# Optimization experiments

Hardware: AMD Instinct MI355X
Metric: run time of the kernel (lower is better)

## Reference

```python
import jax, jax.numpy as jnp
import numpy as np

N = 8192
E = 262144
D_IN = 256
D_OUT = 256
EPS = 1e-05


def setup_inputs() -> dict:
    key = jax.random.key(0)
    kx, ke0, ke1, kw = jax.random.split(key, 4)
    x = jax.random.normal(kx, (N, D_IN), dtype=jnp.float32)
    edge_index = jnp.stack([
        jax.random.randint(ke0, (E,), 0, N, dtype=jnp.int64),
        jax.random.randint(ke1, (E,), 0, N, dtype=jnp.int64),
    ], axis=0)
    # nn.Linear(in, out, bias=False): weight shape [out, in], kaiming-uniform-ish init
    bound = 1.0 / np.sqrt(D_IN)
    W = jax.random.uniform(kw, (D_OUT, D_IN), dtype=jnp.float32, minval=-bound, maxval=bound)
    return {"x": x, "edge_index": edge_index, "W": W}


def reference(x, edge_index, W):
    n = x.shape[0]
    # A_hat = I with edges set to 1 (set semantics; duplicates harmless)
    A_hat = jnp.eye(n, dtype=x.dtype).at[edge_index[0], edge_index[1]].set(1.0)
    # D_hat = diag(1/sqrt(rowsum + eps)); A_norm = D_hat @ A_hat @ D_hat
    d_inv = 1.0 / jnp.sqrt(A_hat.sum(axis=1) + EPS)  # [N]
    A_norm = d_inv[:, None] * A_hat * d_inv[None, :]  # [N, N]
    h = x @ W.T  # [N, D_OUT]
    return jax.nn.relu(A_norm @ h)
```

## Files before the change

kernel.cpp:

```cpp
#include <hip/hip_runtime.h>
#include <hip/hip_bf16.h>
#include <math.h>

#define N_NODES 8192
#define DIM 256
#define WPR 256
#define MAXD 128
#define EPS 1e-5f

typedef __attribute__((ext_vector_type(8))) short bf16x8;
typedef __attribute__((ext_vector_type(4))) float f32x4;

__device__ inline float bfhi(unsigned u) { return __uint_as_float(u & 0xffff0000u); }
__device__ inline float bflo(unsigned u) { return __uint_as_float(u << 16); }

#define NX4 (N_NODES * DIM / 4)
#define NW4 (DIM * DIM / 4)
__global__ __launch_bounds__(256) void prep(const float* __restrict__ x,
                                            const float* __restrict__ W,
                                            const int* __restrict__ erows,
                                            const int* __restrict__ ecols,
                                            __hip_bfloat16* __restrict__ xb,
                                            __hip_bfloat16* __restrict__ Wb,
                                            unsigned* __restrict__ bitmap,
                                            int* __restrict__ degree,
                                            int* __restrict__ cols, int E) {
    int t = blockIdx.x * 256 + threadIdx.x;
    if (t < NX4 + NW4) {
        const float* src = (t < NX4) ? x : W;
        __hip_bfloat16* dst = (t < NX4) ? xb : Wb;
        size_t off = (size_t)((t < NX4) ? t : (t - NX4)) * 4;
        float4 v = *(const float4*)(src + off);
        union { __hip_bfloat16 h[4]; uint2 u; } p;
        p.h[0] = __float2bfloat16(v.x);
        p.h[1] = __float2bfloat16(v.y);
        p.h[2] = __float2bfloat16(v.z);
        p.h[3] = __float2bfloat16(v.w);
        *(uint2*)(dst + off) = p.u;
        return;
    }
    int e = t - (NX4 + NW4);
    if (e >= E + N_NODES) return;
    int r, c;
    if (e < E) { r = erows[e]; c = ecols[e]; }
    else       { r = e - E;    c = r; }
    unsigned bit = 1u << (c & 31);
    unsigned old = atomicOr(&bitmap[(size_t)r * WPR + (c >> 5)], bit);
    if (!(old & bit)) {
        int p = atomicAdd(&degree[r], 1);
        cols[(size_t)r * MAXD + p] = c;
    }
}

__global__ __launch_bounds__(256) void gemm_mfma(const short* __restrict__ xb,
                                                 const short* __restrict__ Wb,
                                                 const int* __restrict__ degree,
                                                 __hip_bfloat16* __restrict__ g) {
    int wave = threadIdx.x >> 6;
    int lane = threadIdx.x & 63;
    int bm = blockIdx.x * 64 + wave * 16;
    int bn = blockIdx.y * 64;
    int quad = lane >> 4;
    int l16 = lane & 15;
    f32x4 acc[4] = {};
    const short* arow = xb + (size_t)(bm + l16) * DIM + quad * 8;
#pragma unroll
    for (int k0 = 0; k0 < DIM; k0 += 32) {
        bf16x8 a = *(const bf16x8*)(arow + k0);
#pragma unroll
        for (int s = 0; s < 4; s++) {
            bf16x8 b = *(const bf16x8*)(Wb + (size_t)(bn + s * 16 + l16) * DIM + k0 + quad * 8);
            acc[s] = __builtin_amdgcn_mfma_f32_16x16x32_bf16(a, b, acc[s], 0, 0, 0);
        }
    }
#pragma unroll
    for (int r = 0; r < 4; r++) {
        int m = bm + quad * 4 + r;
        float s0 = rsqrtf((float)degree[m] + EPS);
#pragma unroll
        for (int s = 0; s < 4; s++)
            g[(size_t)m * DIM + bn + s * 16 + l16] = __float2bfloat16(s0 * acc[s][r]);
    }
}

__global__ __launch_bounds__(256) void aggregate(const int* __restrict__ degree,
                                                 const int* __restrict__ cols,
                                                 const uint2* __restrict__ g2,
                                                 float* __restrict__ out) {
    int wave = threadIdx.x >> 6;
    int lane = threadIdx.x & 63;
    int row = blockIdx.x * 4 + wave;
    int n = degree[row];
    const int* cl = cols + (size_t)row * MAXD;
    float s0[4] = {0.f,0.f,0.f,0.f}, s1[4] = {0.f,0.f,0.f,0.f};
    float s2[4] = {0.f,0.f,0.f,0.f}, s3[4] = {0.f,0.f,0.f,0.f};
    float s4[4] = {0.f,0.f,0.f,0.f}, s5[4] = {0.f,0.f,0.f,0.f};
    float s6[4] = {0.f,0.f,0.f,0.f}, s7[4] = {0.f,0.f,0.f,0.f};
    int i = 0;
    for (; i + 8 <= n; i += 8) {
        int4 ja = *(const int4*)(cl + i);
        int4 jb = *(const int4*)(cl + i + 4);
        uint2 u0 = g2[(size_t)ja.x * 64 + lane];
        uint2 u1 = g2[(size_t)ja.y * 64 + lane];
        uint2 u2 = g2[(size_t)ja.z * 64 + lane];
        uint2 u3 = g2[(size_t)ja.w * 64 + lane];
        uint2 u4 = g2[(size_t)jb.x * 64 + lane];
        uint2 u5 = g2[(size_t)jb.y * 64 + lane];
        uint2 u6 = g2[(size_t)jb.z * 64 + lane];
        uint2 u7 = g2[(size_t)jb.w * 64 + lane];
        s0[0] += bflo(u0.x); s0[1] += bfhi(u0.x); s0[2] += bflo(u0.y); s0[3] += bfhi(u0.y);
        s1[0] += bflo(u1.x); s1[1] += bfhi(u1.x); s1[2] += bflo(u1.y); s1[3] += bfhi(u1.y);
        s2[0] += bflo(u2.x); s2[1] += bfhi(u2.x); s2[2] += bflo(u2.y); s2[3] += bfhi(u2.y);
        s3[0] += bflo(u3.x); s3[1] += bfhi(u3.x); s3[2] += bflo(u3.y); s3[3] += bfhi(u3.y);
        s4[0] += bflo(u4.x); s4[1] += bfhi(u4.x); s4[2] += bflo(u4.y); s4[3] += bfhi(u4.y);
        s5[0] += bflo(u5.x); s5[1] += bfhi(u5.x); s5[2] += bflo(u5.y); s5[3] += bfhi(u5.y);
        s6[0] += bflo(u6.x); s6[1] += bfhi(u6.x); s6[2] += bflo(u6.y); s6[3] += bfhi(u6.y);
        s7[0] += bflo(u7.x); s7[1] += bfhi(u7.x); s7[2] += bflo(u7.y); s7[3] += bfhi(u7.y);
    }
    for (; i + 4 <= n; i += 4) {
        int4 ja = *(const int4*)(cl + i);
        uint2 u0 = g2[(size_t)ja.x * 64 + lane];
        uint2 u1 = g2[(size_t)ja.y * 64 + lane];
        uint2 u2 = g2[(size_t)ja.z * 64 + lane];
        uint2 u3 = g2[(size_t)ja.w * 64 + lane];
        s0[0] += bflo(u0.x); s0[1] += bfhi(u0.x); s0[2] += bflo(u0.y); s0[3] += bfhi(u0.y);
        s1[0] += bflo(u1.x); s1[1] += bfhi(u1.x); s1[2] += bflo(u1.y); s1[3] += bfhi(u1.y);
        s2[0] += bflo(u2.x); s2[1] += bfhi(u2.x); s2[2] += bflo(u2.y); s2[3] += bfhi(u2.y);
        s3[0] += bflo(u3.x); s3[1] += bfhi(u3.x); s3[2] += bflo(u3.y); s3[3] += bfhi(u3.y);
    }
    for (; i < n; i++) {
        uint2 u = g2[(size_t)cl[i] * 64 + lane];
        s0[0] += bflo(u.x); s0[1] += bfhi(u.x); s0[2] += bflo(u.y); s0[3] += bfhi(u.y);
    }
    float sc = rsqrtf((float)n + EPS);
    float4 o;
    o.x = fmaxf(sc * (((s0[0]+s1[0])+(s2[0]+s3[0])) + ((s4[0]+s5[0])+(s6[0]+s7[0]))), 0.f);
    o.y = fmaxf(sc * (((s0[1]+s1[1])+(s2[1]+s3[1])) + ((s4[1]+s5[1])+(s6[1]+s7[1]))), 0.f);
    o.z = fmaxf(sc * (((s0[2]+s1[2])+(s2[2]+s3[2])) + ((s4[2]+s5[2])+(s6[2]+s7[2]))), 0.f);
    o.w = fmaxf(sc * (((s0[3]+s1[3])+(s2[3]+s3[3])) + ((s4[3]+s5[3])+(s6[3]+s7[3]))), 0.f);
    *(float4*)(out + (size_t)row * DIM + lane * 4) = o;
}

extern "C" void kernel_launch(void* const* d_in, const int* in_sizes, int n_in,
                              void* d_out, int out_size, void* d_ws, size_t ws_size,
                              hipStream_t stream) {
    const float* x = (const float*)d_in[0];
    const int* ei = (const int*)d_in[1];
    const float* W = (const float*)d_in[2];
    float* out = (float*)d_out;
    int E = in_sizes[1] / 2;

    unsigned char* ws = (unsigned char*)d_ws;
    size_t off = 0;
    unsigned* bitmap = (unsigned*)(ws + off); off += (size_t)N_NODES * WPR * 4;
    int* degree = (int*)(ws + off);           off += (size_t)N_NODES * 4;
    int* cols = (int*)(ws + off);             off += (size_t)N_NODES * MAXD * 4;
    __hip_bfloat16* xb = (__hip_bfloat16*)(ws + off); off += (size_t)N_NODES * DIM * 2;
    __hip_bfloat16* Wb = (__hip_bfloat16*)(ws + off); off += (size_t)DIM * DIM * 2;
    __hip_bfloat16* g = (__hip_bfloat16*)(ws + off);  off += (size_t)N_NODES * DIM * 2;

    hipMemsetAsync(bitmap, 0, (size_t)N_NODES * WPR * 4 + (size_t)N_NODES * 4, stream);
    int units = NX4 + NW4 + E + N_NODES;
    prep<<<(units + 255) / 256, 256, 0, stream>>>(x, W, ei, ei + E, xb, Wb, bitmap, degree, cols, E);
    dim3 ggrid(N_NODES / 64, DIM / 64);
    gemm_mfma<<<ggrid, 256, 0, stream>>>((const short*)xb, (const short*)Wb, degree, g);
    aggregate<<<N_NODES / 4, 256, 0, stream>>>(degree, cols, (const uint2*)g, out);
}
```

Measured before the change: 118.1 us.

## Fuse bf16 conversion and workspace zeroing into GEMM, move column scaling to aggregate

Replaces the separate memset and the prep kernel's x/W bf16 conversion with a GEMM that converts fp32 tiles to bf16 in shared memory and zeroes the bitmap and degree buffers in a grid-stride loop. Edge scattering becomes its own kernel that runs after the GEMM, so the GEMM no longer needs degree and the source-side normalisation moves into aggregate as a per-neighbour rsqrt FMA. This removes the bf16 copies of x and W and one launch. In exchange, aggregate does extra gathered degree loads and rsqrt work, and the GEMM's conversion is repeated across column blocks.

```diff
diff --git a/kernel.cpp b/kernel.cpp
--- a/kernel.cpp
+++ b/kernel.cpp
@@ -7,6 +7,7 @@
 #define WPR 256
 #define MAXD 128
 #define EPS 1e-5f
+#define ZWORDS (N_NODES * WPR + N_NODES)
 
 typedef __attribute__((ext_vector_type(8))) short bf16x8;
 typedef __attribute__((ext_vector_type(4))) float f32x4;
@@ -14,72 +15,88 @@
 __device__ inline float bfhi(unsigned u) { return __uint_as_float(u & 0xffff0000u); }
 __device__ inline float bflo(unsigned u) { return __uint_as_float(u << 16); }
 
-#define NX4 (N_NODES * DIM / 4)
-#define NW4 (DIM * DIM / 4)
-__global__ __launch_bounds__(256) void prep(const float* __restrict__ x,
-                                            const float* __restrict__ W,
-                                            const int* __restrict__ erows,
-                                            const int* __restrict__ ecols,
-                                            __hip_bfloat16* __restrict__ xb,
-                                            __hip_bfloat16* __restrict__ Wb,
-                                            unsigned* __restrict__ bitmap,
-                                            int* __restrict__ degree,
-                                            int* __restrict__ cols, int E) {
+__device__ inline uint2 pack4(float4 v) {
+    union { __hip_bfloat16 h[4]; uint2 u; } p;
+    p.h[0] = __float2bfloat16(v.x);
+    p.h[1] = __float2bfloat16(v.y);
+    p.h[2] = __float2bfloat16(v.z);
+    p.h[3] = __float2bfloat16(v.w);
+    return p.u;
+}
+
+__global__ __launch_bounds__(256) void gemm_zero(const float* __restrict__ x,
+                                                 const float* __restrict__ W,
+                                                 __hip_bfloat16* __restrict__ g,
+                                                 uint4* __restrict__ zreg) {
+    {
+        const int NZ4 = ZWORDS / 4;
+        int base = (blockIdx.y * 128 + blockIdx.x) * 256 + threadIdx.x;
+        uint4 z = make_uint4(0, 0, 0, 0);
+        for (int i = base; i < NZ4; i += 512 * 256) zreg[i] = z;
+    }
+
+    __shared__ __hip_bfloat16 As[64][136];
+    __shared__ __hip_bfloat16 Bs[64][136];
+    int tid = threadIdx.x;
+    int wave = tid >> 6;
+    int lane = tid & 63;
+    int quad = lane >> 4;
+    int l16 = lane & 15;
+    int bm = blockIdx.x * 64;
+    int bn = blockIdx.y * 64;
+    f32x4 acc[4] = {};
+
+    for (int kb = 0; kb < DIM; kb += 128) {
+        for (int i = tid; i < 64 * 32; i += 256) {
+            int row = i >> 5;
+            int c = (i & 31) * 4;
+            float4 v = *(const float4*)&x[(size_t)(bm + row) * DIM + kb + c];
+            *(uint2*)&As[row][c] = pack4(v);
+            float4 w = *(const float4*)&W[(size_t)(bn + row) * DIM + kb + c];
+            *(uint2*)&Bs[row][c] = pack4(w);
+        }
+        __syncthreads();
+#pragma unroll
+        for (int k0 = 0; k0 < 128; k0 += 32) {
+            bf16x8 a = *(const bf16x8*)&As[wave * 16 + l16][k0 + quad * 8];
+#pragma unroll
+            for (int s = 0; s < 4; s++) {
+                bf16x8 b = *(const bf16x8*)&Bs[s * 16 + l16][k0 + quad * 8];
+                acc[s] = __builtin_amdgcn_mfma_f32_16x16x32_bf16(a, b, acc[s], 0, 0, 0);
+            }
+        }
+        __syncthreads();
+    }
+#pragma unroll
+    for (int r = 0; r < 4; r++) {
+        int m = bm + wave * 16 + quad * 4 + r;
+#pragma unroll
+        for (int s = 0; s < 4; s++)
+            g[(size_t)m * DIM + bn + s * 16 + l16] = __float2bfloat16(acc[s][r]);
+    }
+}
+
+__global__ __launch_bounds__(256) void scatter_all(const int* __restrict__ erows,
+                                                   const int* __restrict__ ecols,
+                                                   unsigned* __restrict__ bitmap,
+                                                   int* __restrict__ degree,
+                                                   int* __restrict__ cols, int E) {
     int t = blockIdx.x * 256 + threadIdx.x;
-    if (t < NX4 + NW4) {
-        const float* src = (t < NX4) ? x : W;
-        __hip_bfloat16* dst = (t < NX4) ? xb : Wb;
-        size_t off = (size_t)((t < NX4) ? t : (t - NX4)) * 4;
-        float4 v = *(const float4*)(src + off);
-        union { __hip_bfloat16 h[4]; uint2 u; } p;
-        p.h[0] = __float2bfloat16(v.x);
-        p.h[1] = __float2bfloat16(v.y);
-        p.h[2] = __float2bfloat16(v.z);
-        p.h[3] = __float2bfloat16(v.w);
-        *(uint2*)(dst + off) = p.u;
+    int r, c;
+    if (t < E) {
+        r = erows[t];
+        c = ecols[t];
+    } else if (t < E + N_NODES) {
+        r = t - E;
+        c = r;
+    } else {
         return;
     }
-    int e = t - (NX4 + NW4);
-    if (e >= E + N_NODES) return;
-    int r, c;
-    if (e < E) { r = erows[e]; c = ecols[e]; }
-    else       { r = e - E;    c = r; }
     unsigned bit = 1u << (c & 31);
     unsigned old = atomicOr(&bitmap[(size_t)r * WPR + (c >> 5)], bit);
     if (!(old & bit)) {
         int p = atomicAdd(&degree[r], 1);
         cols[(size_t)r * MAXD + p] = c;
-    }
-}
-
-__global__ __launch_bounds__(256) void gemm_mfma(const short* __restrict__ xb,
-                                                 const short* __restrict__ Wb,
-                                                 const int* __restrict__ degree,
-                                                 __hip_bfloat16* __restrict__ g) {
-    int wave = threadIdx.x >> 6;
-    int lane = threadIdx.x & 63;
-    int bm = blockIdx.x * 64 + wave * 16;
-    int bn = blockIdx.y * 64;
-    int quad = lane >> 4;
-    int l16 = lane & 15;
-    f32x4 acc[4] = {};
-    const short* arow = xb + (size_t)(bm + l16) * DIM + quad * 8;
-#pragma unroll
-    for (int k0 = 0; k0 < DIM; k0 += 32) {
-        bf16x8 a = *(const bf16x8*)(arow + k0);
-#pragma unroll
-        for (int s = 0; s < 4; s++) {
-            bf16x8 b = *(const bf16x8*)(Wb + (size_t)(bn + s * 16 + l16) * DIM + k0 + quad * 8);
-            acc[s] = __builtin_amdgcn_mfma_f32_16x16x32_bf16(a, b, acc[s], 0, 0, 0);
-        }
-    }
-#pragma unroll
-    for (int r = 0; r < 4; r++) {
-        int m = bm + quad * 4 + r;
-        float s0 = rsqrtf((float)degree[m] + EPS);
-#pragma unroll
-        for (int s = 0; s < 4; s++)
-            g[(size_t)m * DIM + bn + s * 16 + l16] = __float2bfloat16(s0 * acc[s][r]);
     }
 }
 
@@ -100,6 +117,14 @@
     for (; i + 8 <= n; i += 8) {
         int4 ja = *(const int4*)(cl + i);
         int4 jb = *(const int4*)(cl + i + 4);
+        float d0 = rsqrtf((float)degree[ja.x] + EPS);
+        float d1 = rsqrtf((float)degree[ja.y] + EPS);
+        float d2 = rsqrtf((float)degree[ja.z] + EPS);
+        float d3 = rsqrtf((float)degree[ja.w] + EPS);
+        float d4 = rsqrtf((float)degree[jb.x] + EPS);
+        float d5 = rsqrtf((float)degree[jb.y] + EPS);
+        float d6 = rsqrtf((float)degree[jb.z] + EPS);
+        float d7 = rsqrtf((float)degree[jb.w] + EPS);
         uint2 u0 = g2[(size_t)ja.x * 64 + lane];
         uint2 u1 = g2[(size_t)ja.y * 64 + lane];
         uint2 u2 = g2[(size_t)ja.z * 64 + lane];
@@ -108,29 +133,48 @@
         uint2 u5 = g2[(size_t)jb.y * 64 + lane];
         uint2 u6 = g2[(size_t)jb.z * 64 + lane];
         uint2 u7 = g2[(size_t)jb.w * 64 + lane];
-        s0[0] += bflo(u0.x); s0[1] += bfhi(u0.x); s0[2] += bflo(u0.y); s0[3] += bfhi(u0.y);
-        s1[0] += bflo(u1.x); s1[1] += bfhi(u1.x); s1[2] += bflo(u1.y); s1[3] += bfhi(u1.y);
-        s2[0] += bflo(u2.x); s2[1] += bfhi(u2.x); s2[2] += bflo(u2.y); s2[3] += bfhi(u2.y);
-        s3[0] += bflo(u3.x); s3[1] += bfhi(u3.x); s3[2] += bflo(u3.y); s3[3] += bfhi(u3.y);
-        s4[0] += bflo(u4.x); s4[1] += bfhi(u4.x); s4[2] += bflo(u4.y); s4[3] += bfhi(u4.y);
-        s5[0] += bflo(u5.x); s5[1] += bfhi(u5.x); s5[2] += bflo(u5.y); s5[3] += bfhi(u5.y);
-        s6[0] += bflo(u6.x); s6[1] += bfhi(u6.x); s6[2] += bflo(u6.y); s6[3] += bfhi(u6.y);
-        s7[0] += bflo(u7.x); s7[1] += bfhi(u7.x); s7[2] += bflo(u7.y); s7[3] += bfhi(u7.y);
+        s0[0] = fmaf(d0, bflo(u0.x), s0[0]); s0[1] = fmaf(d0, bfhi(u0.x), s0[1]);
+        s0[2] = fmaf(d0, bflo(u0.y), s0[2]); s0[3] = fmaf(d0, bfhi(u0.y), s0[3]);
+        s1[0] = fmaf(d1, bflo(u1.x), s1[0]); s1[1] = fmaf(d1, bfhi(u1.x), s1[1]);
+        s1[2] = fmaf(d1, bflo(u1.y), s1[2]); s1[3] = fmaf(d1, bfhi(u1.y), s1[3]);
+        s2[0] = fmaf(d2, bflo(u2.x), s2[0]); s2[1] = fmaf(d2, bfhi(u2.x), s2[1]);
+        s2[2] = fmaf(d2, bflo(u2.y), s2[2]); s2[3] = fmaf(d2, bfhi(u2.y), s2[3]);
+        s3[0] = fmaf(d3, bflo(u3.x), s3[0]); s3[1] = fmaf(d3, bfhi(u3.x), s3[1]);
+        s3[2] = fmaf(d3, bflo(u3.y), s3[2]); s3[3] = fmaf(d3, bfhi(u3.y), s3[3]);
+        s4[0] = fmaf(d4, bflo(u4.x), s4[0]); s4[1] = fmaf(d4, bfhi(u4.x), s4[1]);
+        s4[2] = fmaf(d4, bflo(u4.y), s4[2]); s4[3] = fmaf(d4, bfhi(u4.y), s4[3]);
+        s5[0] = fmaf(d5, bflo(u5.x), s5[0]); s5[1] = fmaf(d5, bfhi(u5.x), s5[1]);
+        s5[2] = fmaf(d5, bflo(u5.y), s5[2]); s5[3] = fmaf(d5, bfhi(u5.y), s5[3]);
+        s6[0] = fmaf(d6, bflo(u6.x), s6[0]); s6[1] = fmaf(d6, bfhi(u6.x), s6[1]);
+        s6[2] = fmaf(d6, bflo(u6.y), s6[2]); s6[3] = fmaf(d6, bfhi(u6.y), s6[3]);
+        s7[0] = fmaf(d7, bflo(u7.x), s7[0]); s7[1] = fmaf(d7, bfhi(u7.x), s7[1]);
+        s7[2] = fmaf(d7, bflo(u7.y), s7[2]); s7[3] = fmaf(d7, bfhi(u7.y), s7[3]);
     }
     for (; i + 4 <= n; i += 4) {
         int4 ja = *(const int4*)(cl + i);
+        float d0 = rsqrtf((float)degree[ja.x] + EPS);
+        float d1 = rsqrtf((float)degree[ja.y] + EPS);
+        float d2 = rsqrtf((float)degree[ja.z] + EPS);
+        float d3 = rsqrtf((float)degree[ja.w] + EPS);
         uint2 u0 = g2[(size_t)ja.x * 64 + lane];
         uint2 u1 = g2[(size_t)ja.y * 64 + lane];
         uint2 u2 = g2[(size_t)ja.z * 64 + lane];
         uint2 u3 = g2[(size_t)ja.w * 64 + lane];
-        s0[0] += bflo(u0.x); s0[1] += bfhi(u0.x); s0[2] += bflo(u0.y); s0[3] += bfhi(u0.y);
-        s1[0] += bflo(u1.x); s1[1] += bfhi(u1.x); s1[2] += bflo(u1.y); s1[3] += bfhi(u1.y);
-        s2[0] += bflo(u2.x); s2[1] += bfhi(u2.x); s2[2] += bflo(u2.y); s2[3] += bfhi(u2.y);
-        s3[0] += bflo(u3.x); s3[1] += bfhi(u3.x); s3[2] += bflo(u3.y); s3[3] += bfhi(u3.y);
+        s0[0] = fmaf(d0, bflo(u0.x), s0[0]); s0[1] = fmaf(d0, bfhi(u0.x), s0[1]);
+        s0[2] = fmaf(d0, bflo(u0.y), s0[2]); s0[3] = fmaf(d0, bfhi(u0.y), s0[3]);
+        s1[0] = fmaf(d1, bflo(u1.x), s1[0]); s1[1] = fmaf(d1, bfhi(u1.x), s1[1]);
+        s1[2] = fmaf(d1, bflo(u1.y), s1[2]); s1[3] = fmaf(d1, bfhi(u1.y), s1[3]);
+        s2[0] = fmaf(d2, bflo(u2.x), s2[0]); s2[1] = fmaf(d2, bfhi(u2.x), s2[1]);
+        s2[2] = fmaf(d2, bflo(u2.y), s2[2]); s2[3] = fmaf(d2, bfhi(u2.y), s2[3]);
+        s3[0] = fmaf(d3, bflo(u3.x), s3[0]); s3[1] = fmaf(d3, bfhi(u3.x), s3[1]);
+        s3[2] = fmaf(d3, bflo(u3.y), s3[2]); s3[3] = fmaf(d3, bfhi(u3.y), s3[3]);
     }
     for (; i < n; i++) {
-        uint2 u = g2[(size_t)cl[i] * 64 + lane];
-        s0[0] += bflo(u.x); s0[1] += bfhi(u.x); s0[2] += bflo(u.y); s0[3] += bfhi(u.y);
+        int j = cl[i];
+        float d = rsqrtf((float)degree[j] + EPS);
+        uint2 u = g2[(size_t)j * 64 + lane];
+        s0[0] = fmaf(d, bflo(u.x), s0[0]); s0[1] = fmaf(d, bfhi(u.x), s0[1]);
+        s0[2] = fmaf(d, bflo(u.y), s0[2]); s0[3] = fmaf(d, bfhi(u.y), s0[3]);
     }
     float sc = rsqrtf((float)n + EPS);
     float4 o;
@@ -155,14 +199,11 @@
     unsigned* bitmap = (unsigned*)(ws + off); off += (size_t)N_NODES * WPR * 4;
     int* degree = (int*)(ws + off);           off += (size_t)N_NODES * 4;
     int* cols = (int*)(ws + off);             off += (size_t)N_NODES * MAXD * 4;
-    __hip_bfloat16* xb = (__hip_bfloat16*)(ws + off); off += (size_t)N_NODES * DIM * 2;
-    __hip_bfloat16* Wb = (__hip_bfloat16*)(ws + off); off += (size_t)DIM * DIM * 2;
-    __hip_bfloat16* g = (__hip_bfloat16*)(ws + off);  off += (size_t)N_NODES * DIM * 2;
-
-    hipMemsetAsync(bitmap, 0, (size_t)N_NODES * WPR * 4 + (size_t)N_NODES * 4, stream);
-    int units = NX4 + NW4 + E + N_NODES;
-    prep<<<(units + 255) / 256, 256, 0, stream>>>(x, W, ei, ei + E, xb, Wb, bitmap, degree, cols, E);
+    __hip_bfloat16* g = (__hip_bfloat16*)(ws + off); off += (size_t)N_NODES * DIM * 2;
+
     dim3 ggrid(N_NODES / 64, DIM / 64);
-    gemm_mfma<<<ggrid, 256, 0, stream>>>((const short*)xb, (const short*)Wb, degree, g);
+    gemm_zero<<<ggrid, 256, 0, stream>>>(x, W, g, (uint4*)bitmap);
+    int total = E + N_NODES;
+    scatter_all<<<(total + 255) / 256, 256, 0, stream>>>(ei, ei + E, bitmap, degree, cols, E);
     aggregate<<<N_NODES / 4, 256, 0, stream>>>(degree, cols, (const uint2*)g, out);
 }
```

New measurement: 116.4 us. About the same (-1.4%).
